# Kernel optimization log

Measured on AMD Instinct MI355X. Metric: run time of the kernel, lower is better.

The kernel has to match this reference:

```python
import jax, jax.numpy as jnp
import numpy as np

GRID = (15, 15)
HW = GRID[0] * GRID[1]
IMAGE_SIZE = 240
TEMP = 0.07
EPS = 1e-12


def make_masks(h, w, k):
    grid = np.arange(h * w).reshape(h, w)
    # matches torch unfold: kernel offsets row-major, spatial positions row-major
    idx = np.stack([grid[i:i + h - k + 1, j:j + w - k + 1] for i in range(k) for j in range(k)])
    return jnp.asarray(idx.reshape(k * k, -1), dtype=jnp.int32)  # [k*k, n_masks]


def _l2n(x):
    return x / jnp.maximum(jnp.linalg.norm(x, axis=-1, keepdims=True), EPS)


def cosine_sim(a, b):
    # a: [..., N, D], b: [M, D] -> [..., N, M]
    return jnp.einsum('...nd,md->...nm', _l2n(a), _l2n(b))


def harmonic_aggregation(window_scores, masks):
    # window_scores: [B, n_masks]; masks: [k2, n_masks] flat patch indices
    n_masks = masks.shape[1]
    # membership matrix M[p, w] = 1 if patch p is covered by window w
    M = jnp.zeros((HW, n_masks), dtype=window_scores.dtype)
    M = M.at[masks, jnp.arange(n_masks)[None, :]].set(1.0)
    counts = M.sum(axis=1)                                  # [HW]
    sums = (1.0 / window_scores) @ M.T                      # [B, HW]
    scores = counts[None, :] / sums
    scores = jnp.nan_to_num(scores, nan=0.0, posinf=0.0)
    return scores.reshape(-1, GRID[0], GRID[1])


def visual_association_score(embeds, ref_embeds):
    # embeds: [B, N, D]; ref_embeds: [K, N, D]
    flat = ref_embeds.reshape(-1, embeds.shape[-1])          # [K*N, D]
    scores = cosine_sim(embeds, flat)                        # [B, N, K*N]
    return (1.0 - scores).min(axis=-1) / 2.0                 # [B, N]


def setup_inputs() -> dict:
    key = jax.random.key(0)
    ks = jax.random.split(key, 8)
    B, D, K = 256, 640, 4
    return {
        'image_embeds': jax.random.normal(ks[0], (B, D), jnp.float32),
        'window_embeds_s2': jax.random.normal(ks[1], (B, 196, D), jnp.float32),
        'window_embeds_s3': jax.random.normal(ks[2], (B, 169, D), jnp.float32),
        'patch_embeds': jax.random.normal(ks[3], (B, 225, D), jnp.float32),
        'text_embeds': jax.random.normal(ks[4], (2, D), jnp.float32),
        'ref_patch_embeds': jax.random.normal(ks[5], (K, 225, D), jnp.float32),
        'ref_window_s2': jax.random.normal(ks[6], (K, 196, D), jnp.float32),
        'ref_window_s3': jax.random.normal(ks[7], (K, 169, D), jnp.float32),
        'masks_s2': make_masks(GRID[0], GRID[1], 2),
        'masks_s3': make_masks(GRID[0], GRID[1], 3),
    }


def reference(image_embeds, window_embeds_s2, window_embeds_s3, patch_embeds,
              text_embeds, ref_patch_embeds, ref_window_s2, ref_window_s3,
              masks_s2, masks_s3):
    B = image_embeds.shape[0]
    # image-level zero-shot anomaly score
    img_probs = jax.nn.softmax(cosine_sim(image_embeds, text_embeds) / TEMP, axis=-1)
    image_scores = img_probs[..., 1]                         # [B]

    # zero-shot multi-scale (harmonic mean of image score + window scores)
    zs = [jnp.broadcast_to(image_scores[:, None, None], (B, GRID[0], GRID[1]))]
    for we, m in ((window_embeds_s2, masks_s2), (window_embeds_s3, masks_s3)):
        s = jax.nn.softmax(cosine_sim(we, text_embeds) / TEMP, axis=-1)[..., 1]  # [B, n_masks]
        zs.append(harmonic_aggregation(s, m))
    zero_shot = len(zs) / (1.0 / jnp.stack(zs)).sum(axis=0)   # [B, H, W]

    # few-shot scores
    fs = [visual_association_score(patch_embeds, ref_patch_embeds).reshape(B, GRID[0], GRID[1])]
    for we, re, m in ((window_embeds_s2, ref_window_s2, masks_s2),
                      (window_embeds_s3, ref_window_s3, masks_s3)):
        fs.append(harmonic_aggregation(visual_association_score(we, re), m))
    few_shot = jnp.stack(fs).mean(axis=0)                     # [B, H, W]

    multi_scale = (zero_shot + few_shot) / 2.0
    image_scores = (image_scores + few_shot.max(axis=(-2, -1))) / 2.0
    pixel_scores = jax.image.resize(multi_scale, (B, IMAGE_SIZE, IMAGE_SIZE), method='bilinear')
    return image_scores, pixel_scores
```

## Files before the change

kernel.cpp:

```cpp
#include <hip/hip_runtime.h>
#include <cmath>

#define D 640
#define TEMP_INV (1.0f / 0.07f)

typedef __attribute__((ext_vector_type(8))) short bf16x8;
typedef __attribute__((ext_vector_type(4))) float f32x4;

__device__ __forceinline__ short f2bf(float f) {
    unsigned int u = __float_as_uint(f);
    unsigned int r = (u + 0x7fffu + ((u >> 16) & 1u)) >> 16;
    return (short)r;
}

__device__ __forceinline__ void gload_lds16(const void* g, void* l) {
    __builtin_amdgcn_global_load_lds(
        (const __attribute__((address_space(1))) unsigned int*)g,
        (__attribute__((address_space(3))) unsigned int*)l, 16, 0, 0);
}

__global__ void textnorm_k(const float* __restrict__ T, float* __restrict__ tn) {
    int w = threadIdx.x >> 6, lane = threadIdx.x & 63;
    const float* row = T + w * D;
    float v[10]; float ss = 0.f;
#pragma unroll
    for (int i = 0; i < 10; i++) { v[i] = row[lane + 64 * i]; ss += v[i] * v[i]; }
#pragma unroll
    for (int m = 1; m < 64; m <<= 1) ss += __shfl_xor(ss, m, 64);
    float rn = 1.f / fmaxf(sqrtf(ss), 1e-12f);
#pragma unroll
    for (int i = 0; i < 10; i++) tn[w * D + lane + 64 * i] = v[i] * rn;
}

__global__ __launch_bounds__(256) void normstore_k(
    const float* __restrict__ X, int nsrc, int npad, const float* __restrict__ tn,
    float* __restrict__ score_out, short* __restrict__ bf16_out) {
    int wid = blockIdx.x * 4 + (threadIdx.x >> 6);
    int lane = threadIdx.x & 63;
    if (wid >= npad) return;
    const float2* row = (const float2*)(X + (size_t)(wid < nsrc ? wid : 0) * D);
    const float2* t0 = (const float2*)tn;
    const float2* t1 = (const float2*)(tn + D);
    float2 v[5]; float ss = 0.f, d0 = 0.f, d1 = 0.f;
#pragma unroll
    for (int i = 0; i < 5; i++) {
        float2 a = row[lane + 64 * i];
        v[i] = a;
        ss += a.x * a.x + a.y * a.y;
        if (tn) {
            float2 b0 = t0[lane + 64 * i], b1 = t1[lane + 64 * i];
            d0 += a.x * b0.x + a.y * b0.y;
            d1 += a.x * b1.x + a.y * b1.y;
        }
    }
#pragma unroll
    for (int m = 1; m < 64; m <<= 1) {
        ss += __shfl_xor(ss, m, 64);
        if (tn) { d0 += __shfl_xor(d0, m, 64); d1 += __shfl_xor(d1, m, 64); }
    }
    float rn = 1.f / fmaxf(sqrtf(ss), 1e-12f);
    if (score_out && lane == 0)
        score_out[wid] = 1.f / (1.f + expf(-((d1 - d0) * rn) * TEMP_INV));
    if (bf16_out) {
        ushort2* o = (ushort2*)bf16_out;
#pragma unroll
        for (int i = 0; i < 5; i++) {
            ushort2 p;
            p.x = (unsigned short)f2bf(v[i].x * rn);
            p.y = (unsigned short)f2bf(v[i].y * rn);
            o[(size_t)wid * 320 + lane + 64 * i] = p;
        }
    }
}

__global__ __launch_bounds__(256, 4) void gemm_max_k(
    const short* __restrict__ A, const short* __restrict__ B,
    int nch, int U, float* __restrict__ partial) {
    __shared__ short Al[128 * 64];
    __shared__ short Bl[128 * 64];
    const int t = threadIdx.x;
    const int g = blockIdx.x & 7, ii = blockIdx.x >> 3;
    const int ulo = (int)(((long long)g * U) >> 3);
    const int uhi = (int)(((long long)(g + 1) * U) >> 3);
    const int u = ulo + ii;
    if (u >= uhi) return;
    const int rc = u / nch, nc = u - rc * nch;
    const int nchq = nch * 2;

    const int srow = t >> 3;
    const int scol = (t & 7) * 16;
    const int gsw = (scol ^ ((srow & 7) << 4)) >> 1;

    const int lane = t & 63, wave = t >> 6;
    const int l15 = lane & 15, lhi = lane >> 4;
    const int wr = wave >> 1, wc = wave & 1;
    const int xk = (l15 & 7) << 4;

    char* Ab = (char*)Al;
    char* Bb = (char*)Bl;
    char* Ad = Ab + t * 16;
    char* Bd = Bb + t * 16;

    const short* Ag = A + ((size_t)rc * 128 + srow) * D + gsw;
    const short* Bg = B + ((size_t)nc * 128 + srow) * D + gsw;

    f32x4 acc[4][4];
#pragma unroll
    for (int m = 0; m < 4; m++)
#pragma unroll
        for (int n = 0; n < 4; n++) acc[m][n] = (f32x4){0.f, 0.f, 0.f, 0.f};

    for (int ks = 0; ks < 10; ks++) {
        const int k0 = ks * 64;
        __syncthreads();
#pragma unroll
        for (int i = 0; i < 4; i++)
            gload_lds16(Ag + k0 + (size_t)(i * 32) * D, Ad + i * 4096);
#pragma unroll
        for (int i = 0; i < 4; i++)
            gload_lds16(Bg + k0 + (size_t)(i * 32) * D, Bd + i * 4096);
        __syncthreads();
        __builtin_amdgcn_s_setprio(1);
#pragma unroll
        for (int sub = 0; sub < 2; sub++) {
            const int kbs = (sub * 64 + lhi * 16) ^ xk;
            bf16x8 a[4], b[4];
#pragma unroll
            for (int m = 0; m < 4; m++)
                a[m] = *(const bf16x8*)(Ab + (wr * 64 + m * 16 + l15) * 128 + kbs);
#pragma unroll
            for (int n = 0; n < 4; n++)
                b[n] = *(const bf16x8*)(Bb + (wc * 64 + n * 16 + l15) * 128 + kbs);
#pragma unroll
            for (int m = 0; m < 4; m++)
#pragma unroll
                for (int n = 0; n < 4; n++)
                    acc[m][n] = __builtin_amdgcn_mfma_f32_16x16x32_bf16(a[m], b[n], acc[m][n], 0, 0, 0);
        }
        __builtin_amdgcn_s_setprio(0);
    }

#pragma unroll
    for (int m = 0; m < 4; m++)
#pragma unroll
        for (int r = 0; r < 4; r++) {
            float v = fmaxf(fmaxf(acc[m][0][r], acc[m][1][r]),
                            fmaxf(acc[m][2][r], acc[m][3][r]));
#pragma unroll
            for (int msk = 1; msk < 16; msk <<= 1)
                v = fmaxf(v, __shfl_xor(v, msk, 64));
            if (l15 == 0) {
                int row = rc * 128 + wr * 64 + m * 16 + lhi * 4 + r;
                partial[(size_t)row * nchq + nc * 2 + wc] = v;
            }
        }
}

__global__ __launch_bounds__(256) void reducemax_k(
    const float* __restrict__ partial, int nchq, int nrows, float* __restrict__ vas) {
    int r = blockIdx.x * 256 + threadIdx.x;
    if (r >= nrows) return;
    float m = -1e30f;
    for (int i = 0; i < nchq; i++) m = fmaxf(m, partial[(size_t)r * nchq + i]);
    vas[r] = (1.0f - m) * 0.5f;
}

__global__ __launch_bounds__(256) void rowstats_k(
    const float* __restrict__ X, int nrows, const float* __restrict__ tn,
    float* __restrict__ rnorm_out, float* __restrict__ score_out) {
    int wid = blockIdx.x * 4 + (threadIdx.x >> 6);
    int lane = threadIdx.x & 63;
    if (wid >= nrows) return;
    const float* row = X + (size_t)wid * D;
    float ss = 0.f, d0 = 0.f, d1 = 0.f;
#pragma unroll
    for (int i = 0; i < 10; i++) {
        float v = row[lane + 64 * i];
        ss += v * v;
        if (tn) { d0 += v * tn[lane + 64 * i]; d1 += v * tn[D + lane + 64 * i]; }
    }
#pragma unroll
    for (int m = 1; m < 64; m <<= 1) {
        ss += __shfl_xor(ss, m, 64);
        if (tn) { d0 += __shfl_xor(d0, m, 64); d1 += __shfl_xor(d1, m, 64); }
    }
    if (lane == 0) {
        float rn = 1.f / fmaxf(sqrtf(ss), 1e-12f);
        if (rnorm_out) rnorm_out[wid] = rn;
        if (score_out) score_out[wid] = 1.f / (1.f + expf(-((d1 - d0) * rn) * TEMP_INV));
    }
}

__global__ __launch_bounds__(256) void refnorm_k(
    const float* __restrict__ R, int M, int Mp, short* __restrict__ out) {
    int wid = blockIdx.x * 4 + (threadIdx.x >> 6);
    int lane = threadIdx.x & 63;
    if (wid >= Mp) return;
    const float* row = R + (size_t)(wid < M ? wid : 0) * D;
    float v[10]; float ss = 0.f;
#pragma unroll
    for (int i = 0; i < 10; i++) { v[i] = row[lane + 64 * i]; ss += v[i] * v[i]; }
#pragma unroll
    for (int m = 1; m < 64; m <<= 1) ss += __shfl_xor(ss, m, 64);
    float rn = 1.f / fmaxf(sqrtf(ss), 1e-12f);
#pragma unroll
    for (int i = 0; i < 10; i++) out[(size_t)wid * D + lane + 64 * i] = f2bf(v[i] * rn);
}

#define SA 648
#define SB 72
__global__ __launch_bounds__(256) void maxcos_k(
    const float* __restrict__ X, const float* __restrict__ rnorm,
    const short* __restrict__ refs, int Mp, float* __restrict__ vas_out) {
    __shared__ short Alds[64 * SA];
    __shared__ short Blds[64 * SB];
    const int t = threadIdx.x;
    const size_t rowBase = (size_t)blockIdx.x * 64;
#pragma unroll
    for (int i = 0; i < 20; i++) {
        int c = i * 256 + t;
        int row = c / 80, col = (c % 80) * 8;
        const float* p = X + (rowBase + row) * D + col;
        float rn = rnorm[rowBase + row];
        float4 v0 = *(const float4*)p;
        float4 v1 = *(const float4*)(p + 4);
        bf16x8 s;
        s[0] = f2bf(v0.x * rn); s[1] = f2bf(v0.y * rn);
        s[2] = f2bf(v0.z * rn); s[3] = f2bf(v0.w * rn);
        s[4] = f2bf(v1.x * rn); s[5] = f2bf(v1.y * rn);
        s[6] = f2bf(v1.z * rn); s[7] = f2bf(v1.w * rn);
        *(bf16x8*)&Alds[row * SA + col] = s;
    }
    __syncthreads();
    const int lane = t & 63, wave = t >> 6;
    const int l15 = lane & 15, lhi = lane >> 4;
    const int wr0 = wave * 16;
    float rowmax[4] = {-1e30f, -1e30f, -1e30f, -1e30f};
    for (int m0 = 0; m0 < Mp; m0 += 64) {
        f32x4 zero = {0.f, 0.f, 0.f, 0.f};
        f32x4 acc[4] = {zero, zero, zero, zero};
        for (int ks = 0; ks < 10; ks++) {
            __syncthreads();
#pragma unroll
            for (int c2 = 0; c2 < 2; c2++) {
                int c = c2 * 256 + t;
                int n = c >> 3, kk = (c & 7) * 8;
                const short* g = refs + (size_t)(m0 + n) * D + ks * 64 + kk;
                *(bf16x8*)&Blds[n * SB + kk] = *(const bf16x8*)g;
            }
            __syncthreads();
#pragma unroll
            for (int sub = 0; sub < 2; sub++) {
                bf16x8 a = *(const bf16x8*)&Alds[(wr0 + l15) * SA + ks * 64 + sub * 32 + lhi * 8];
#pragma unroll
                for (int s = 0; s < 4; s++) {
                    bf16x8 b = *(const bf16x8*)&Blds[(s * 16 + l15) * SB + sub * 32 + lhi * 8];
                    acc[s] = __builtin_amdgcn_mfma_f32_16x16x32_bf16(a, b, acc[s], 0, 0, 0);
                }
            }
        }
#pragma unroll
        for (int r = 0; r < 4; r++) {
            float mv = fmaxf(fmaxf(acc[0][r], acc[1][r]), fmaxf(acc[2][r], acc[3][r]));
#pragma unroll
            for (int msk = 1; msk < 16; msk <<= 1) mv = fmaxf(mv, __shfl_xor(mv, msk, 64));
            rowmax[r] = fmaxf(rowmax[r], mv);
        }
    }
    if (l15 == 0) {
#pragma unroll
        for (int r = 0; r < 4; r++) {
            size_t row = rowBase + wr0 + lhi * 4 + r;
            vas_out[row] = (1.0f - rowmax[r]) * 0.5f;
        }
    }
}

__global__ __launch_bounds__(256) void fuse_k(
    const float* __restrict__ imgsc, const float* __restrict__ zs2,
    const float* __restrict__ zs3, const float* __restrict__ vasP,
    const float* __restrict__ vas2, const float* __restrict__ vas3,
    float* __restrict__ multi, float* __restrict__ img_out) {
    int b = blockIdx.x, t = threadIdx.x;
    __shared__ float red[256];
    float few = -1e30f;
    if (t < 225) {
        int i = t / 15, j = t % 15;
        float invz2 = 0.f, invf2 = 0.f; int c2 = 0;
        int ilo = max(0, i - 1), ihi = min(i, 13), jlo = max(0, j - 1), jhi = min(j, 13);
        for (int i0 = ilo; i0 <= ihi; i0++)
            for (int j0 = jlo; j0 <= jhi; j0++) {
                int w = b * 196 + i0 * 14 + j0;
                invz2 += 1.f / zs2[w]; invf2 += 1.f / vas2[w]; c2++;
            }
        float zh2 = (float)c2 / invz2, fh2 = (float)c2 / invf2;
        float invz3 = 0.f, invf3 = 0.f; int c3 = 0;
        ilo = max(0, i - 2); ihi = min(i, 12); jlo = max(0, j - 2); jhi = min(j, 12);
        for (int i0 = ilo; i0 <= ihi; i0++)
            for (int j0 = jlo; j0 <= jhi; j0++) {
                int w = b * 169 + i0 * 13 + j0;
                invz3 += 1.f / zs3[w]; invf3 += 1.f / vas3[w]; c3++;
            }
        float zh3 = (float)c3 / invz3, fh3 = (float)c3 / invf3;
        float is = imgsc[b];
        float zero_shot = 3.f / (1.f / is + 1.f / zh2 + 1.f / zh3);
        float fs0 = vasP[b * 225 + t];
        few = (fs0 + fh2 + fh3) * (1.f / 3.f);
        multi[b * 225 + t] = (zero_shot + few) * 0.5f;
    }
    red[t] = few;
    __syncthreads();
    for (int s = 128; s > 0; s >>= 1) {
        if (t < s) red[t] = fmaxf(red[t], red[t + s]);
        __syncthreads();
    }
    if (t == 0) img_out[b] = (imgsc[b] + red[0]) * 0.5f;
}

__global__ __launch_bounds__(256) void resize_k(
    const float* __restrict__ multi, float* __restrict__ out) {
    int idx = blockIdx.x * 256 + threadIdx.x;
    int x = idx % 240;
    int rest = idx / 240;
    int y = rest % 240;
    int b = rest / 240;
    float sx = (x + 0.5f) * 0.0625f - 0.5f;
    float sy = (y + 0.5f) * 0.0625f - 0.5f;
    sx = fminf(fmaxf(sx, 0.f), 14.f);
    sy = fminf(fmaxf(sy, 0.f), 14.f);
    int x0 = min((int)sx, 13), y0 = min((int)sy, 13);
    float fx = sx - x0, fy = sy - y0;
    const float* m = multi + b * 225;
    float v00 = m[y0 * 15 + x0],      v01 = m[y0 * 15 + x0 + 1];
    float v10 = m[y0 * 15 + 15 + x0], v11 = m[y0 * 15 + 15 + x0 + 1];
    out[idx] = (1.f - fy) * ((1.f - fx) * v00 + fx * v01)
             + fy * ((1.f - fx) * v10 + fx * v11);
}

extern "C" void kernel_launch(void* const* d_in, const int* in_sizes, int n_in,
                              void* d_out, int out_size, void* d_ws, size_t ws_size,
                              hipStream_t stream) {
    const float* image = (const float*)d_in[0];
    const float* w2    = (const float*)d_in[1];
    const float* w3    = (const float*)d_in[2];
    const float* patch = (const float*)d_in[3];
    const float* text  = (const float*)d_in[4];
    const float* refP  = (const float*)d_in[5];
    const float* ref2  = (const float*)d_in[6];
    const float* ref3  = (const float*)d_in[7];
    float* out_img = (float*)d_out;
    float* out_pix = out_img + 256;

    char* wsb = (char*)d_ws;
    size_t off = 0;
    auto alloc = [&](size_t bytes) -> void* {
        void* p = wsb + off;
        off += (bytes + 255) & ~(size_t)255;
        return p;
    };

    const size_t NEW_NEED = 72300000;
    if (ws_size >= NEW_NEED) {
        float* tn    = (float*)alloc(2 * 640 * 4);
        float* imgsc = (float*)alloc(256 * 4);
        float* zs2   = (float*)alloc(50176 * 4);
        float* zs3   = (float*)alloc(43264 * 4);
        short* nrefP = (short*)alloc(1024 * 640 * 2);
        short* nref2 = (short*)alloc(896 * 640 * 2);
        short* nref3 = (short*)alloc(768 * 640 * 2);
        short* Abuf  = (short*)alloc((size_t)50176 * 640 * 2);
        float* partial = (float*)alloc((size_t)50176 * 16 * 4);
        float* vasP  = (float*)alloc(57600 * 4);
        float* vas2  = (float*)alloc(50176 * 4);
        float* vas3  = (float*)alloc(43264 * 4);
        float* multi = (float*)alloc(57600 * 4);

        textnorm_k<<<1, 128, 0, stream>>>(text, tn);
        normstore_k<<<64, 256, 0, stream>>>(image, 256, 256, tn, imgsc, nullptr);
        normstore_k<<<256, 256, 0, stream>>>(refP, 900, 1024, nullptr, nullptr, nrefP);
        normstore_k<<<224, 256, 0, stream>>>(ref2, 784, 896, nullptr, nullptr, nref2);
        normstore_k<<<192, 256, 0, stream>>>(ref3, 676, 768, nullptr, nullptr, nref3);

        for (int h = 0; h < 2; h++) {
            const float* src = patch + (size_t)h * 28800 * D;
            normstore_k<<<7200, 256, 0, stream>>>(src, 28800, 28800, nullptr, nullptr, Abuf);
            gemm_max_k<<<1800, 256, 0, stream>>>(Abuf, nrefP, 8, 1800, partial);
            reducemax_k<<<113, 256, 0, stream>>>(partial, 16, 28800, vasP + h * 28800);
        }
        normstore_k<<<12544, 256, 0, stream>>>(w2, 50176, 50176, tn, zs2, Abuf);
        gemm_max_k<<<2744, 256, 0, stream>>>(Abuf, nref2, 7, 2744, partial);
        reducemax_k<<<196, 256, 0, stream>>>(partial, 14, 50176, vas2);
        normstore_k<<<10816, 256, 0, stream>>>(w3, 43264, 43264, tn, zs3, Abuf);
        gemm_max_k<<<2032, 256, 0, stream>>>(Abuf, nref3, 6, 2028, partial);
        reducemax_k<<<169, 256, 0, stream>>>(partial, 12, 43264, vas3);

        fuse_k<<<256, 256, 0, stream>>>(imgsc, zs2, zs3, vasP, vas2, vas3, multi, out_img);
        resize_k<<<57600, 256, 0, stream>>>(multi, out_pix);
    } else {
        float* tn    = (float*)alloc(2 * 640 * 4);
        float* imgsc = (float*)alloc(256 * 4);
        float* rn2   = (float*)alloc(50176 * 4);
        float* rn3   = (float*)alloc(43264 * 4);
        float* rnp   = (float*)alloc(57600 * 4);
        float* zs2   = (float*)alloc(50176 * 4);
        float* zs3   = (float*)alloc(43264 * 4);
        short* nrefP = (short*)alloc(960 * 640 * 2);
        short* nref2 = (short*)alloc(832 * 640 * 2);
        short* nref3 = (short*)alloc(704 * 640 * 2);
        float* vasP  = (float*)alloc(57600 * 4);
        float* vas2  = (float*)alloc(50176 * 4);
        float* vas3  = (float*)alloc(43264 * 4);
        float* multi = (float*)alloc(57600 * 4);

        textnorm_k<<<1, 128, 0, stream>>>(text, tn);
        rowstats_k<<<64, 256, 0, stream>>>(image, 256, tn, nullptr, imgsc);
        rowstats_k<<<12544, 256, 0, stream>>>(w2, 50176, tn, rn2, zs2);
        rowstats_k<<<10816, 256, 0, stream>>>(w3, 43264, tn, rn3, zs3);
        rowstats_k<<<14400, 256, 0, stream>>>(patch, 57600, nullptr, rnp, nullptr);
        refnorm_k<<<240, 256, 0, stream>>>(refP, 900, 960, nrefP);
        refnorm_k<<<208, 256, 0, stream>>>(ref2, 784, 832, nref2);
        refnorm_k<<<176, 256, 0, stream>>>(ref3, 676, 704, nref3);
        maxcos_k<<<900, 256, 0, stream>>>(patch, rnp, nrefP, 960, vasP);
        maxcos_k<<<784, 256, 0, stream>>>(w2, rn2, nref2, 832, vas2);
        maxcos_k<<<676, 256, 0, stream>>>(w3, rn3, nref3, 704, vas3);
        fuse_k<<<256, 256, 0, stream>>>(imgsc, zs2, zs3, vasP, vas2, vas3, multi, out_img);
        resize_k<<<57600, 256, 0, stream>>>(multi, out_pix);
    }
}
```

Baseline: 382.9 us.

## Fuse patch normalization and bf16 conversion into the max-GEMM kernel

For the patch-embedding branch, the separate normstore pass that wrote normalized bf16 rows is removed. A new GEMM kernel reads raw fp32 rows, converts them to bf16 on the fly into LDS, and accumulates the squared norm along the way. The row norm is applied after the max inside reducemax, which holds because a positive per-row scale commutes with max. This removes one full read/write pass over the patch tensor, but each GEMM block now rereads fp32 A data (twice the bytes) for every N-chunk, and the A tile is loaded synchronously rather than through global_load_lds.

```diff
diff --git a/kernel.cpp b/kernel.cpp
--- a/kernel.cpp
+++ b/kernel.cpp
@@ -1,4 +1,5 @@
 #include <hip/hip_runtime.h>
+#include <hip/hip_bf16.h>
 #include <cmath>
 
 #define D 640
@@ -11,6 +12,11 @@
     unsigned int u = __float_as_uint(f);
     unsigned int r = (u + 0x7fffu + ((u >> 16) & 1u)) >> 16;
     return (short)r;
+}
+
+__device__ __forceinline__ short f2bf_hw(float f) {
+    __hip_bfloat16 h = __float2bfloat16(f);
+    return *reinterpret_cast<short*>(&h);
 }
 
 __device__ __forceinline__ void gload_lds16(const void* g, void* l) {
@@ -156,13 +162,116 @@
         }
 }
 
+__global__ __launch_bounds__(256, 4) void gemm_maxraw_k(
+    const float* __restrict__ Araw, const short* __restrict__ B,
+    int nch, int U, float* __restrict__ partial, float* __restrict__ grnorm) {
+    __shared__ short Al[128 * 64];
+    __shared__ short Bl[128 * 64];
+    const int t = threadIdx.x;
+    const int g = blockIdx.x & 7, ii = blockIdx.x >> 3;
+    const int ulo = (int)(((long long)g * U) >> 3);
+    const int uhi = (int)(((long long)(g + 1) * U) >> 3);
+    const int u = ulo + ii;
+    if (u >= uhi) return;
+    const int rc = u / nch, nc = u - rc * nch;
+    const int nchq = nch * 2;
+
+    const int srow = t >> 3;
+    const int scol = (t & 7) * 16;
+    const int gsw = (scol ^ ((srow & 7) << 4)) >> 1;
+    const int arow = t >> 1;
+    const int acb  = (t & 1) * 32;
+    const int aswz = (arow & 7) << 4;
+
+    const int lane = t & 63, wave = t >> 6;
+    const int l15 = lane & 15, lhi = lane >> 4;
+    const int wr = wave >> 1, wc = wave & 1;
+    const int xk = (l15 & 7) << 4;
+
+    char* Ab = (char*)Al;
+    char* Bb = (char*)Bl;
+    char* Bd = Bb + t * 16;
+    char* Awr = Ab + arow * 128;
+
+    const short* Bg = B + ((size_t)nc * 128 + srow) * D + gsw;
+    const float* Ag = Araw + ((size_t)rc * 128 + arow) * D + acb;
+
+    float ss = 0.f;
+    f32x4 acc[4][4];
+#pragma unroll
+    for (int m = 0; m < 4; m++)
+#pragma unroll
+        for (int n = 0; n < 4; n++) acc[m][n] = (f32x4){0.f, 0.f, 0.f, 0.f};
+
+    for (int ks = 0; ks < 10; ks++) {
+        const int k0 = ks * 64;
+        __syncthreads();
+#pragma unroll
+        for (int i = 0; i < 4; i++)
+            gload_lds16(Bg + k0 + (size_t)(i * 32) * D, Bd + i * 4096);
+#pragma unroll
+        for (int j = 0; j < 4; j++) {
+            float4 v0 = *(const float4*)(Ag + k0 + j * 8);
+            float4 v1 = *(const float4*)(Ag + k0 + j * 8 + 4);
+            ss += v0.x * v0.x + v0.y * v0.y + v0.z * v0.z + v0.w * v0.w
+                + v1.x * v1.x + v1.y * v1.y + v1.z * v1.z + v1.w * v1.w;
+            bf16x8 pk;
+            pk[0] = f2bf_hw(v0.x); pk[1] = f2bf_hw(v0.y);
+            pk[2] = f2bf_hw(v0.z); pk[3] = f2bf_hw(v0.w);
+            pk[4] = f2bf_hw(v1.x); pk[5] = f2bf_hw(v1.y);
+            pk[6] = f2bf_hw(v1.z); pk[7] = f2bf_hw(v1.w);
+            *(bf16x8*)(Awr + ((acb * 2 + j * 16) ^ aswz)) = pk;
+        }
+        __syncthreads();
+        __builtin_amdgcn_s_setprio(1);
+#pragma unroll
+        for (int sub = 0; sub < 2; sub++) {
+            const int kbs = (sub * 64 + lhi * 16) ^ xk;
+            bf16x8 a[4], b[4];
+#pragma unroll
+            for (int m = 0; m < 4; m++)
+                a[m] = *(const bf16x8*)(Ab + (wr * 64 + m * 16 + l15) * 128 + kbs);
+#pragma unroll
+            for (int n = 0; n < 4; n++)
+                b[n] = *(const bf16x8*)(Bb + (wc * 64 + n * 16 + l15) * 128 + kbs);
+#pragma unroll
+            for (int m = 0; m < 4; m++)
+#pragma unroll
+                for (int n = 0; n < 4; n++)
+                    acc[m][n] = __builtin_amdgcn_mfma_f32_16x16x32_bf16(a[m], b[n], acc[m][n], 0, 0, 0);
+        }
+        __builtin_amdgcn_s_setprio(0);
+    }
+
+    ss += __shfl_xor(ss, 1, 64);
+    if (nc == 0 && (t & 1) == 0)
+        grnorm[rc * 128 + arow] = 1.f / fmaxf(sqrtf(ss), 1e-12f);
+
+#pragma unroll
+    for (int m = 0; m < 4; m++)
+#pragma unroll
+        for (int r = 0; r < 4; r++) {
+            float v = fmaxf(fmaxf(acc[m][0][r], acc[m][1][r]),
+                            fmaxf(acc[m][2][r], acc[m][3][r]));
+#pragma unroll
+            for (int msk = 1; msk < 16; msk <<= 1)
+                v = fmaxf(v, __shfl_xor(v, msk, 64));
+            if (l15 == 0) {
+                int row = rc * 128 + wr * 64 + m * 16 + lhi * 4 + r;
+                partial[(size_t)row * nchq + nc * 2 + wc] = v;
+            }
+        }
+}
+
 __global__ __launch_bounds__(256) void reducemax_k(
-    const float* __restrict__ partial, int nchq, int nrows, float* __restrict__ vas) {
+    const float* __restrict__ partial, int nchq, int nrows,
+    const float* __restrict__ rnorm, float* __restrict__ vas) {
     int r = blockIdx.x * 256 + threadIdx.x;
     if (r >= nrows) return;
     float m = -1e30f;
     for (int i = 0; i < nchq; i++) m = fmaxf(m, partial[(size_t)r * nchq + i]);
-    vas[r] = (1.0f - m) * 0.5f;
+    float s = rnorm ? rnorm[r] : 1.f;
+    vas[r] = (1.0f - s * m) * 0.5f;
 }
 
 __global__ __launch_bounds__(256) void rowstats_k(
@@ -359,7 +468,7 @@
         return p;
     };
 
-    const size_t NEW_NEED = 72300000;
+    const size_t NEW_NEED = 72500000;
     if (ws_size >= NEW_NEED) {
         float* tn    = (float*)alloc(2 * 640 * 4);
         float* imgsc = (float*)alloc(256 * 4);
@@ -370,6 +479,7 @@
         short* nref3 = (short*)alloc(768 * 640 * 2);
         short* Abuf  = (short*)alloc((size_t)50176 * 640 * 2);
         float* partial = (float*)alloc((size_t)50176 * 16 * 4);
+        float* grnorm  = (float*)alloc(28800 * 4);
         float* vasP  = (float*)alloc(57600 * 4);
         float* vas2  = (float*)alloc(50176 * 4);
         float* vas3  = (float*)alloc(43264 * 4);
@@ -383,16 +493,15 @@
 
         for (int h = 0; h < 2; h++) {
             const float* src = patch + (size_t)h * 28800 * D;
-            normstore_k<<<7200, 256, 0, stream>>>(src, 28800, 28800, nullptr, nullptr, Abuf);
-            gemm_max_k<<<1800, 256, 0, stream>>>(Abuf, nrefP, 8, 1800, partial);
-            reducemax_k<<<113, 256, 0, stream>>>(partial, 16, 28800, vasP + h * 28800);
+            gemm_maxraw_k<<<1800, 256, 0, stream>>>(src, nrefP, 8, 1800, partial, grnorm);
+            reducemax_k<<<113, 256, 0, stream>>>(partial, 16, 28800, grnorm, vasP + h * 28800);
         }
         normstore_k<<<12544, 256, 0, stream>>>(w2, 50176, 50176, tn, zs2, Abuf);
         gemm_max_k<<<2744, 256, 0, stream>>>(Abuf, nref2, 7, 2744, partial);
-        reducemax_k<<<196, 256, 0, stream>>>(partial, 14, 50176, vas2);
+        reducemax_k<<<196, 256, 0, stream>>>(partial, 14, 50176, nullptr, vas2);
         normstore_k<<<10816, 256, 0, stream>>>(w3, 43264, 43264, tn, zs3, Abuf);
         gemm_max_k<<<2032, 256, 0, stream>>>(Abuf, nref3, 6, 2028, partial);
-        reducemax_k<<<169, 256, 0, stream>>>(partial, 12, 43264, vas3);
+        reducemax_k<<<169, 256, 0, stream>>>(partial, 12, 43264, nullptr, vas3);
 
         fuse_k<<<256, 256, 0, stream>>>(imgsc, zs2, zs3, vasP, vas2, vas3, multi, out_img);
         resize_k<<<57600, 256, 0, stream>>>(multi, out_pix);
```

Result: slower. 480.1 us (+25.4%).
